# Kernel optimization log

Hardware: AMD Instinct MI355X
Metric: run time of the kernel (lower is better)

The kernel has to match this reference:

```python
import jax, jax.numpy as jnp
import numpy as np

N_NODES = 100000
N_EDGES = 3200000
F_IN = 128
HIDDEN = 16
OUT_DIM = 16
NUM_GRAPHS = 64


def setup_inputs() -> dict:
    key = jax.random.key(0)
    ks = jax.random.split(key, 9)
    x = jax.random.normal(ks[0], (N_NODES, F_IN), dtype=jnp.float32)
    edge_index = jax.random.randint(ks[1], (2, N_EDGES), 0, N_NODES, dtype=jnp.int32)
    batch = jnp.sort(jax.random.randint(ks[2], (N_NODES,), 0, NUM_GRAPHS, dtype=jnp.int32))
    W1 = jax.random.normal(ks[3], (F_IN, HIDDEN), dtype=jnp.float32) * (1.0 / np.sqrt(F_IN))
    b1 = jnp.zeros((HIDDEN,), dtype=jnp.float32)
    W2 = jax.random.normal(ks[4], (HIDDEN, OUT_DIM), dtype=jnp.float32) * (1.0 / np.sqrt(HIDDEN))
    b2 = jnp.zeros((OUT_DIM,), dtype=jnp.float32)
    fc_w = jax.random.normal(ks[5], (OUT_DIM, 1), dtype=jnp.float32) * (1.0 / np.sqrt(OUT_DIM))
    fc_b = jnp.zeros((1,), dtype=jnp.float32)
    return {"x": x, "edge_index": edge_index, "batch": batch,
            "W1": W1, "b1": b1, "W2": W2, "b2": b2, "fc_w": fc_w, "fc_b": fc_b}


def _gcn_conv(x, edge_index, W, b):
    """PyG GCNConv: x' = D^-1/2 (A+I) D^-1/2 (x W) + b (with self-loops)."""
    n = x.shape[0]
    h = x @ W  # transform first (small dim), then propagate
    src, dst = edge_index[0], edge_index[1]
    # degree including the self-loop (+1)
    deg = jax.ops.segment_sum(jnp.ones(src.shape, h.dtype), dst, num_segments=n) + 1.0
    dis = jax.lax.rsqrt(deg)  # deg >= 1 so no zeros
    norm = dis[src] * dis[dst]  # [E]
    agg = jax.ops.segment_sum(h[src] * norm[:, None], dst, num_segments=n)
    # self-loop contribution: norm_ii = dis[i]^2
    return agg + (dis * dis)[:, None] * h + b


def reference(x, edge_index, batch, W1, b1, W2, b2, fc_w, fc_b):
    h = jax.nn.relu(_gcn_conv(x, edge_index, W1, b1))
    # F.dropout(training=False) in eval mode is identity
    h = jax.nn.relu(_gcn_conv(h, edge_index, W2, b2))
    pooled = jax.ops.segment_sum(h, batch, num_segments=NUM_GRAPHS)  # global_add_pool
    return jax.nn.sigmoid(pooled @ fc_w + fc_b)  # [NUM_GRAPHS, 1]
```

## Files before the change

### kernel.cpp

```cpp
#include <hip/hip_runtime.h>
#include <hip/hip_fp16.h>
#include <math.h>

#define N_NODES 100000
#define N_EDGES 3200000
#define F_IN    128
#define NGRAPH  64

#define NB      512
#define BWIDTH  196
#define NPAD    100352
#define BIN_CAP 7200
#define EPB     4096

typedef int   iv4 __attribute__((ext_vector_type(4)));
typedef float fv4 __attribute__((ext_vector_type(4)));
typedef float fv2 __attribute__((ext_vector_type(2)));

#define OFF_BINCUR 0
#define OFF_GZ     512
#define OFF_BBASE  576
#define OFF_DIS    1088
#define OFF_ROWR   (1088 + NPAD)
#define OFF_COL    (1088 + NPAD * 3)
#define OFF_BINNED (OFF_COL + N_EDGES)
#define OFF_HINH   OFF_BINNED
#define OFF_HINH2  (OFF_BINNED + NPAD * 8)

__global__ void zero_k(int* __restrict__ p) {
    p[threadIdx.x] = 0;
}

__global__ void __launch_bounds__(512)
bin_k(const int* __restrict__ ei, int* __restrict__ binCursor,
      int* __restrict__ binned) {
    __shared__ int cntL[NB], cnt2[NB], gbase[NB];
    int tid = threadIdx.x;
    cntL[tid] = 0; cnt2[tid] = 0;
    __syncthreads();
    int myBase = blockIdx.x * EPB + tid * 8;
    bool act = (myBase < N_EDGES);
    int s[8], d[8];
    if (act) {
        const iv4* sp = (const iv4*)(ei + myBase);
        const iv4* dp = (const iv4*)(ei + N_EDGES + myBase);
        iv4 a = __builtin_nontemporal_load(sp);
        iv4 b2 = __builtin_nontemporal_load(sp + 1);
        iv4 c = __builtin_nontemporal_load(dp);
        iv4 e = __builtin_nontemporal_load(dp + 1);
        s[0]=a.x; s[1]=a.y; s[2]=a.z; s[3]=a.w; s[4]=b2.x; s[5]=b2.y; s[6]=b2.z; s[7]=b2.w;
        d[0]=c.x; d[1]=c.y; d[2]=c.z; d[3]=c.w; d[4]=e.x; d[5]=e.y; d[6]=e.z; d[7]=e.w;
#pragma unroll
        for (int k = 0; k < 8; ++k)
            atomicAdd(&cntL[(unsigned)d[k] / BWIDTH], 1);
    }
    __syncthreads();
    gbase[tid] = atomicAdd(&binCursor[tid], cntL[tid]);
    __syncthreads();
    if (act) {
#pragma unroll
        for (int k = 0; k < 8; ++k) {
            int b = (unsigned)d[k] / BWIDTH;
            int off = atomicAdd(&cnt2[b], 1);
            binned[(size_t)b * BIN_CAP + gbase[b] + off] = ((d[k] - b * BWIDTH) << 17) | s[k];
        }
    }
}

__global__ void __launch_bounds__(512)
scanB_k(const int* __restrict__ binCur, int* __restrict__ bucketBase) {
    __shared__ int wsum[8];
    int tid = threadIdx.x;
    int v = binCur[tid];
    int lane = tid & 63, wid = tid >> 6;
    int sc = v;
#pragma unroll
    for (int d = 1; d < 64; d <<= 1) {
        int o = __shfl_up(sc, d);
        if (lane >= d) sc += o;
    }
    if (lane == 63) wsum[wid] = sc;
    __syncthreads();
    int woff = 0;
    for (int w = 0; w < wid; ++w) woff += wsum[w];
    bucketBase[tid] = woff + sc - v;
}

__global__ void __launch_bounds__(512)
sort_k(const int* __restrict__ binCursor, const int* __restrict__ bucketBase,
       const int* __restrict__ binned, float* __restrict__ dis,
       int2* __restrict__ rowRange, int* __restrict__ col) {
    __shared__ int cnt[BWIDTH];
    __shared__ int rowLoc[BWIDTH + 1];
    __shared__ int cur[BWIDTH];
    __shared__ int wsum[8];
    int b = blockIdx.x, tid = threadIdx.x;
    if (tid < BWIDTH) cnt[tid] = 0;
    __syncthreads();
    int n = binCursor[b];
    const int* bb = binned + (size_t)b * BIN_CAP;
    for (int i = tid; i < n; i += 512)
        atomicAdd(&cnt[bb[i] >> 17], 1);
    __syncthreads();
    int base = b * BWIDTH;
    int bw = min(BWIDTH, N_NODES - base);
    if (tid < bw)
        dis[base + tid] = rsqrtf((float)cnt[tid] + 1.0f);
    int a = (tid < BWIDTH) ? cnt[tid] : 0;
    int lane = tid & 63, wid = tid >> 6;
    int sc = a;
#pragma unroll
    for (int d = 1; d < 64; d <<= 1) {
        int o = __shfl_up(sc, d);
        if (lane >= d) sc += o;
    }
    if (lane == 63) wsum[wid] = sc;
    __syncthreads();
    int woff = 0;
    for (int w = 0; w < wid; ++w) woff += wsum[w];
    if (tid < BWIDTH) {
        int excl = woff + sc - a;
        rowLoc[tid] = excl;
        cur[tid] = excl;
    }
    if (tid == 0) rowLoc[BWIDTH] = n;
    __syncthreads();
    int eb = bucketBase[b];
    if (tid < bw) {
        int2 rr; rr.x = eb + rowLoc[tid]; rr.y = eb + rowLoc[tid + 1];
        rowRange[base + tid] = rr;
    }
    for (int i = tid; i < n; i += 512) {
        int p = bb[i];
        int pos = atomicAdd(&cur[p >> 17], 1);
        col[eb + pos] = p & 0x1FFFF;
    }
}

__global__ void transform1_k(const float* __restrict__ x, const float* __restrict__ W,
                             const float* __restrict__ dis, __half* __restrict__ outh) {
    int i = blockIdx.x * blockDim.x + threadIdx.x;
    if (i >= N_NODES) return;
    const fv4* xr = (const fv4*)(x + (size_t)i * F_IN);
    float acc[16];
#pragma unroll
    for (int j = 0; j < 16; ++j) acc[j] = 0.f;
#pragma unroll 4
    for (int k4 = 0; k4 < F_IN / 4; ++k4) {
        fv4 xv = xr[k4];
#pragma unroll
        for (int kk = 0; kk < 4; ++kk) {
            int k = k4 * 4 + kk;
            float xk = xv[kk];
#pragma unroll
            for (int j = 0; j < 16; ++j)
                acc[j] = fmaf(xk, W[k * 16 + j], acc[j]);
        }
    }
    float di = dis[i];
    __half2 t[8];
#pragma unroll
    for (int q = 0; q < 8; ++q)
        t[q] = __floats2half2_rn(di * acc[2 * q], di * acc[2 * q + 1]);
    iv4* o = (iv4*)(outh + (size_t)i * 16);
    o[0] = *(iv4*)&t[0];
    o[1] = *(iv4*)&t[4];
}

__device__ __forceinline__ void gather_row(const __half2* __restrict__ hh,
                                           const int* __restrict__ col,
                                           int e0, int e1, int j,
                                           float& outx, float& outy) {
    float ax0 = 0.f, ay0 = 0.f, ax1 = 0.f, ay1 = 0.f;
    float ax2 = 0.f, ay2 = 0.f, ax3 = 0.f, ay3 = 0.f;
    float bx0 = 0.f, by0 = 0.f, bx1 = 0.f, by1 = 0.f;
    float bx2 = 0.f, by2 = 0.f, bx3 = 0.f, by3 = 0.f;
    int e = e0;
    for (; e + 8 <= e1; e += 8) {
        int myc = col[e + j];
        int s0 = __shfl(myc, 0, 8);
        int s1 = __shfl(myc, 1, 8);
        int s2 = __shfl(myc, 2, 8);
        int s3 = __shfl(myc, 3, 8);
        int s4 = __shfl(myc, 4, 8);
        int s5 = __shfl(myc, 5, 8);
        int s6 = __shfl(myc, 6, 8);
        int s7 = __shfl(myc, 7, 8);
        float2 f0 = __half22float2(hh[s0 * 8 + j]);
        float2 f1 = __half22float2(hh[s1 * 8 + j]);
        float2 f2 = __half22float2(hh[s2 * 8 + j]);
        float2 f3 = __half22float2(hh[s3 * 8 + j]);
        float2 f4 = __half22float2(hh[s4 * 8 + j]);
        float2 f5 = __half22float2(hh[s5 * 8 + j]);
        float2 f6 = __half22float2(hh[s6 * 8 + j]);
        float2 f7 = __half22float2(hh[s7 * 8 + j]);
        ax0 += f0.x; ay0 += f0.y;
        ax1 += f1.x; ay1 += f1.y;
        ax2 += f2.x; ay2 += f2.y;
        ax3 += f3.x; ay3 += f3.y;
        bx0 += f4.x; by0 += f4.y;
        bx1 += f5.x; by1 += f5.y;
        bx2 += f6.x; by2 += f6.y;
        bx3 += f7.x; by3 += f7.y;
    }
    if (e + 4 <= e1) {
        int myc = col[e + (j & 3)];
        int s0 = __shfl(myc, 0, 8);
        int s1 = __shfl(myc, 1, 8);
        int s2 = __shfl(myc, 2, 8);
        int s3 = __shfl(myc, 3, 8);
        float2 f0 = __half22float2(hh[s0 * 8 + j]);
        float2 f1 = __half22float2(hh[s1 * 8 + j]);
        float2 f2 = __half22float2(hh[s2 * 8 + j]);
        float2 f3 = __half22float2(hh[s3 * 8 + j]);
        ax0 += f0.x; ay0 += f0.y;
        ax1 += f1.x; ay1 += f1.y;
        ax2 += f2.x; ay2 += f2.y;
        ax3 += f3.x; ay3 += f3.y;
        e += 4;
    }
    for (; e < e1; ++e) {
        float2 f = __half22float2(hh[col[e] * 8 + j]);
        ax0 += f.x; ay0 += f.y;
    }
    outx = ((ax0 + ax1) + (ax2 + ax3)) + ((bx0 + bx1) + (bx2 + bx3));
    outy = ((ay0 + ay1) + (ay2 + ay3)) + ((by0 + by1) + (by2 + by3));
}

__global__ void prop1_k(const __half* __restrict__ hinh, const float* __restrict__ dis,
                        const int2* __restrict__ rowRange, const int* __restrict__ col,
                        const float* __restrict__ b1, const float* __restrict__ W2,
                        __half* __restrict__ outh2) {
    int gid = blockIdx.x * blockDim.x + threadIdx.x;
    int node = gid >> 3;
    int j = gid & 7;
    if (node >= N_NODES) return;
    int2 rr = rowRange[node];
    const __half2* hh = (const __half2*)hinh;
    float sx, sy;
    gather_row(hh, col, rr.x, rr.y, j, sx, sy);
    float2 self = __half22float2(hh[node * 8 + j]);
    float di = dis[node];
    fv2 bj = ((const fv2*)b1)[j];
    float hx = fmaxf(fmaf(di, sx + self.x, bj.x), 0.f);
    float hy = fmaxf(fmaf(di, sy + self.y, bj.y), 0.f);
    float h1[16];
#pragma unroll
    for (int k = 0; k < 8; ++k) {
        h1[2 * k]     = __shfl(hx, k, 8);
        h1[2 * k + 1] = __shfl(hy, k, 8);
    }
    const fv2* w2 = (const fv2*)W2;
    float o0 = 0.f, o1 = 0.f;
#pragma unroll
    for (int m = 0; m < 16; ++m) {
        fv2 wv = w2[m * 8 + j];
        o0 = fmaf(h1[m], wv.x, o0);
        o1 = fmaf(h1[m], wv.y, o1);
    }
    ((__half2*)outh2)[node * 8 + j] = __floats2half2_rn(di * o0, di * o1);
}

__global__ void __launch_bounds__(256)
prop2_k(const __half* __restrict__ hinh2, const float* __restrict__ dis,
        const int2* __restrict__ rowRange, const int* __restrict__ col,
        const float* __restrict__ b2, const int* __restrict__ batch,
        const float* __restrict__ fcw, float* __restrict__ gz) {
    __shared__ float ldsz[NGRAPH];
    int tid = threadIdx.x;
    if (tid < NGRAPH) ldsz[tid] = 0.f;
    __syncthreads();
    int gid = blockIdx.x * 256 + tid;
    int node = gid >> 3;
    int j = gid & 7;
    int2 rr = rowRange[node];
    const __half2* hh = (const __half2*)hinh2;
    float sx, sy;
    gather_row(hh, col, rr.x, rr.y, j, sx, sy);
    float2 self = __half22float2(hh[node * 8 + j]);
    float di = dis[node];
    fv2 bj = ((const fv2*)b2)[j];
    float hx = fmaxf(fmaf(di, sx + self.x, bj.x), 0.f);
    float hy = fmaxf(fmaf(di, sy + self.y, bj.y), 0.f);
    fv2 fw = ((const fv2*)fcw)[j];
    float s = hx * fw.x + hy * fw.y;
#pragma unroll
    for (int off = 4; off; off >>= 1) s += __shfl_xor(s, off, 8);
    if (j == 0) atomicAdd(&ldsz[batch[node]], s);
    __syncthreads();
    if (tid < NGRAPH) {
        float v = ldsz[tid];
        if (v != 0.f) atomicAdd(&gz[tid], v);
    }
}

__global__ void sig_k(const float* __restrict__ gz, const float* __restrict__ fcb,
                      float* __restrict__ out) {
    int g = threadIdx.x;
    out[g] = 1.0f / (1.0f + expf(-(gz[g] + fcb[0])));
}

extern "C" void kernel_launch(void* const* d_in, const int* in_sizes, int n_in,
                              void* d_out, int out_size, void* d_ws, size_t ws_size,
                              hipStream_t stream) {
    const float* x    = (const float*)d_in[0];
    const int*   ei   = (const int*)d_in[1];
    const int*   batch= (const int*)d_in[2];
    const float* W1   = (const float*)d_in[3];
    const float* b1   = (const float*)d_in[4];
    const float* W2   = (const float*)d_in[5];
    const float* b2   = (const float*)d_in[6];
    const float* fcw  = (const float*)d_in[7];
    const float* fcb  = (const float*)d_in[8];
    float* out = (float*)d_out;

    float* ws = (float*)d_ws;
    int*    binCur   = (int*)(ws + OFF_BINCUR);
    float*  gz       = ws + OFF_GZ;
    int*    bucketBase = (int*)(ws + OFF_BBASE);
    float*  dis      = ws + OFF_DIS;
    int2*   rowRange = (int2*)(ws + OFF_ROWR);
    int*    col      = (int*)(ws + OFF_COL);
    int*    binned   = (int*)(ws + OFF_BINNED);
    __half* hinH     = (__half*)(ws + OFF_HINH);
    __half* hinH2    = (__half*)(ws + OFF_HINH2);

    const int B = 256;
    int gN   = (N_NODES + B - 1) / B;
    int gNP  = (N_NODES * 8 + B - 1) / B;
    int gBin = (N_EDGES + EPB - 1) / EPB;

    zero_k<<<1, 576, 0, stream>>>(binCur);
    bin_k<<<gBin, 512, 0, stream>>>(ei, binCur, binned);
    scanB_k<<<1, 512, 0, stream>>>(binCur, bucketBase);
    sort_k<<<NB, 512, 0, stream>>>(binCur, bucketBase, binned, dis, rowRange, col);

    transform1_k<<<gN, B, 0, stream>>>(x, W1, dis, hinH);
    prop1_k<<<gNP, B, 0, stream>>>(hinH, dis, rowRange, col, b1, W2, hinH2);
    prop2_k<<<gNP, B, 0, stream>>>(hinH2, dis, rowRange, col, b2, batch, fcw, gz);
    sig_k<<<1, NGRAPH, 0, stream>>>(gz, fcb, out);
}
```

Measured before the change: 148.9 us.

## Sort nodes by degree within windows to balance gather work per wavefront

Records per-node in-degree in the sort kernel and adds a windowed counting-sort kernel that builds a permutation grouping nodes of similar degree within 2048-node windows. Both propagation kernels process nodes through this permutation so the eight nodes sharing a wavefront have similar neighbor counts, reducing idle lanes in the gather loop. It adds a kernel launch, an extra indirection load, and less contiguous access to per-node arrays and output rows.

```diff
diff --git a/kernel.cpp b/kernel.cpp
--- a/kernel.cpp
+++ b/kernel.cpp
@@ -12,6 +12,7 @@
 #define NPAD    100352
 #define BIN_CAP 7200
 #define EPB     4096
+#define PWIN    2048
 
 typedef int   iv4 __attribute__((ext_vector_type(4)));
 typedef float fv4 __attribute__((ext_vector_type(4)));
@@ -21,8 +22,10 @@
 #define OFF_GZ     512
 #define OFF_BBASE  576
 #define OFF_DIS    1088
-#define OFF_ROWR   (1088 + NPAD)
-#define OFF_COL    (1088 + NPAD * 3)
+#define OFF_DEG    (1088 + NPAD)
+#define OFF_PERM   (1088 + NPAD * 2)
+#define OFF_ROWR   (1088 + NPAD * 3)
+#define OFF_COL    (1088 + NPAD * 5)
 #define OFF_BINNED (OFF_COL + N_EDGES)
 #define OFF_HINH   OFF_BINNED
 #define OFF_HINH2  (OFF_BINNED + NPAD * 8)
@@ -89,7 +92,7 @@
 __global__ void __launch_bounds__(512)
 sort_k(const int* __restrict__ binCursor, const int* __restrict__ bucketBase,
        const int* __restrict__ binned, float* __restrict__ dis,
-       int2* __restrict__ rowRange, int* __restrict__ col) {
+       int* __restrict__ deg, int2* __restrict__ rowRange, int* __restrict__ col) {
     __shared__ int cnt[BWIDTH];
     __shared__ int rowLoc[BWIDTH + 1];
     __shared__ int cur[BWIDTH];
@@ -104,8 +107,10 @@
     __syncthreads();
     int base = b * BWIDTH;
     int bw = min(BWIDTH, N_NODES - base);
-    if (tid < bw)
+    if (tid < bw) {
         dis[base + tid] = rsqrtf((float)cnt[tid] + 1.0f);
+        deg[base + tid] = cnt[tid];
+    }
     int a = (tid < BWIDTH) ? cnt[tid] : 0;
     int lane = tid & 63, wid = tid >> 6;
     int sc = a;
@@ -134,6 +139,42 @@
         int p = bb[i];
         int pos = atomicAdd(&cur[p >> 17], 1);
         col[eb + pos] = p & 0x1FFFF;
+    }
+}
+
+__global__ void __launch_bounds__(512)
+permW_k(const int* __restrict__ deg, int* __restrict__ perm) {
+    __shared__ int hist[128];
+    int w0 = blockIdx.x * PWIN;
+    int wn = min(PWIN, N_NODES - w0);
+    int tid = threadIdx.x;
+    if (tid < 128) hist[tid] = 0;
+    __syncthreads();
+    int mybin[4];
+#pragma unroll
+    for (int k = 0; k < 4; ++k) {
+        int i = tid * 4 + k;
+        mybin[k] = -1;
+        if (i < wn) {
+            int d = min(deg[w0 + i], 127);
+            mybin[k] = d;
+            atomicAdd(&hist[d], 1);
+        }
+    }
+    __syncthreads();
+    if (tid == 0) {
+        int acc = 0;
+#pragma unroll
+        for (int bN = 0; bN < 128; ++bN) { int c = hist[bN]; hist[bN] = acc; acc += c; }
+    }
+    __syncthreads();
+#pragma unroll
+    for (int k = 0; k < 4; ++k) {
+        int i = tid * 4 + k;
+        if (i < wn) {
+            int pos = atomicAdd(&hist[mybin[k]], 1);
+            perm[w0 + pos] = w0 + i;
+        }
     }
 }
 
@@ -229,12 +270,14 @@
 
 __global__ void prop1_k(const __half* __restrict__ hinh, const float* __restrict__ dis,
                         const int2* __restrict__ rowRange, const int* __restrict__ col,
+                        const int* __restrict__ perm,
                         const float* __restrict__ b1, const float* __restrict__ W2,
                         __half* __restrict__ outh2) {
     int gid = blockIdx.x * blockDim.x + threadIdx.x;
-    int node = gid >> 3;
+    int grp = gid >> 3;
     int j = gid & 7;
-    if (node >= N_NODES) return;
+    if (grp >= N_NODES) return;
+    int node = perm[grp];
     int2 rr = rowRange[node];
     const __half2* hh = (const __half2*)hinh;
     float sx, sy;
@@ -264,6 +307,7 @@
 __global__ void __launch_bounds__(256)
 prop2_k(const __half* __restrict__ hinh2, const float* __restrict__ dis,
         const int2* __restrict__ rowRange, const int* __restrict__ col,
+        const int* __restrict__ perm,
         const float* __restrict__ b2, const int* __restrict__ batch,
         const float* __restrict__ fcw, float* __restrict__ gz) {
     __shared__ float ldsz[NGRAPH];
@@ -271,8 +315,9 @@
     if (tid < NGRAPH) ldsz[tid] = 0.f;
     __syncthreads();
     int gid = blockIdx.x * 256 + tid;
-    int node = gid >> 3;
+    int grp = gid >> 3;
     int j = gid & 7;
+    int node = perm[grp];
     int2 rr = rowRange[node];
     const __half2* hh = (const __half2*)hinh2;
     float sx, sy;
@@ -319,6 +364,8 @@
     float*  gz       = ws + OFF_GZ;
     int*    bucketBase = (int*)(ws + OFF_BBASE);
     float*  dis      = ws + OFF_DIS;
+    int*    deg      = (int*)(ws + OFF_DEG);
+    int*    perm     = (int*)(ws + OFF_PERM);
     int2*   rowRange = (int2*)(ws + OFF_ROWR);
     int*    col      = (int*)(ws + OFF_COL);
     int*    binned   = (int*)(ws + OFF_BINNED);
@@ -329,14 +376,16 @@
     int gN   = (N_NODES + B - 1) / B;
     int gNP  = (N_NODES * 8 + B - 1) / B;
     int gBin = (N_EDGES + EPB - 1) / EPB;
+    int gPW  = (N_NODES + PWIN - 1) / PWIN;
 
     zero_k<<<1, 576, 0, stream>>>(binCur);
     bin_k<<<gBin, 512, 0, stream>>>(ei, binCur, binned);
     scanB_k<<<1, 512, 0, stream>>>(binCur, bucketBase);
-    sort_k<<<NB, 512, 0, stream>>>(binCur, bucketBase, binned, dis, rowRange, col);
+    sort_k<<<NB, 512, 0, stream>>>(binCur, bucketBase, binned, dis, deg, rowRange, col);
+    permW_k<<<gPW, 512, 0, stream>>>(deg, perm);
 
     transform1_k<<<gN, B, 0, stream>>>(x, W1, dis, hinH);
-    prop1_k<<<gNP, B, 0, stream>>>(hinH, dis, rowRange, col, b1, W2, hinH2);
-    prop2_k<<<gNP, B, 0, stream>>>(hinH2, dis, rowRange, col, b2, batch, fcw, gz);
+    prop1_k<<<gNP, B, 0, stream>>>(hinH, dis, rowRange, col, perm, b1, W2, hinH2);
+    prop2_k<<<gNP, B, 0, stream>>>(hinH2, dis, rowRange, col, perm, b2, batch, fcw, gz);
     sig_k<<<1, NGRAPH, 0, stream>>>(gz, fcb, out);
 }
```

Result: slower. 156.9 us (+5.3%).

## Reorder nodes by degree within each bin to balance gather workloads

Applied to the files above, without the earlier changes.

The sort kernel now counting-sorts the nodes of each 196-node bin by in-degree, then emits a permuted row-range array and a nodeOf map. Both propagation kernels walk this permuted order, so the 8-lane groups in a wavefront handle nodes of similar degree. This is meant to cut lane divergence and tail imbalance in the gather loops. In exchange it adds extra LDS passes and barriers in sort_k, an extra indirection load per node, and less locality in the self-feature and dis accesses.

```diff
diff --git a/kernel.cpp b/kernel.cpp
--- a/kernel.cpp
+++ b/kernel.cpp
@@ -21,8 +21,9 @@
 #define OFF_GZ     512
 #define OFF_BBASE  576
 #define OFF_DIS    1088
-#define OFF_ROWR   (1088 + NPAD)
-#define OFF_COL    (1088 + NPAD * 3)
+#define OFF_NODEOF (1088 + NPAD)
+#define OFF_ROWR   (1088 + NPAD * 2)
+#define OFF_COL    (1088 + NPAD * 4)
 #define OFF_BINNED (OFF_COL + N_EDGES)
 #define OFF_HINH   OFF_BINNED
 #define OFF_HINH2  (OFF_BINNED + NPAD * 8)
@@ -89,13 +90,17 @@
 __global__ void __launch_bounds__(512)
 sort_k(const int* __restrict__ binCursor, const int* __restrict__ bucketBase,
        const int* __restrict__ binned, float* __restrict__ dis,
-       int2* __restrict__ rowRange, int* __restrict__ col) {
+       int* __restrict__ nodeOf, int2* __restrict__ rowRangeP, int* __restrict__ col) {
     __shared__ int cnt[BWIDTH];
-    __shared__ int rowLoc[BWIDTH + 1];
+    __shared__ int rank[BWIDTH];
+    __shared__ int nodeOfRank[BWIDTH];
+    __shared__ int rowLoc[BWIDTH];
     __shared__ int cur[BWIDTH];
+    __shared__ int histD[128];
     __shared__ int wsum[8];
     int b = blockIdx.x, tid = threadIdx.x;
     if (tid < BWIDTH) cnt[tid] = 0;
+    if (tid >= 256 && tid < 384) histD[tid - 256] = 0;
     __syncthreads();
     int n = binCursor[b];
     const int* bb = binned + (size_t)b * BIN_CAP;
@@ -103,33 +108,65 @@
         atomicAdd(&cnt[bb[i] >> 17], 1);
     __syncthreads();
     int base = b * BWIDTH;
-    int bw = min(BWIDTH, N_NODES - base);
-    if (tid < bw)
-        dis[base + tid] = rsqrtf((float)cnt[tid] + 1.0f);
-    int a = (tid < BWIDTH) ? cnt[tid] : 0;
-    int lane = tid & 63, wid = tid >> 6;
+    int bw = N_NODES - base;
+    if (bw > BWIDTH) bw = BWIDTH;
+    if (bw < 0) bw = 0;
+    int myDeg = (tid < bw) ? cnt[tid] : 0;
+    int myBin = myDeg > 127 ? 127 : myDeg;
+    if (tid < bw) {
+        dis[base + tid] = rsqrtf((float)myDeg + 1.0f);
+        atomicAdd(&histD[myBin], 1);
+    }
+    __syncthreads();
+    {
+        int hv = (tid < 128) ? histD[tid] : 0;
+        int lane = tid & 63, wid = tid >> 6;
+        int sc = hv;
+#pragma unroll
+        for (int d = 1; d < 64; d <<= 1) {
+            int o = __shfl_up(sc, d);
+            if (lane >= d) sc += o;
+        }
+        if (lane == 63 && wid < 2) wsum[wid] = sc;
+        __syncthreads();
+        if (tid < 128) {
+            int woff = (wid == 1) ? wsum[0] : 0;
+            histD[tid] = woff + sc - hv;
+        }
+    }
+    __syncthreads();
+    if (tid < bw) rank[tid] = atomicAdd(&histD[myBin], 1);
+    __syncthreads();
+    if (tid < bw) nodeOfRank[rank[tid]] = tid;
+    __syncthreads();
+    int a = (tid < bw) ? cnt[nodeOfRank[tid]] : 0;
+    int lane = tid & 63, wid2 = tid >> 6;
     int sc = a;
 #pragma unroll
     for (int d = 1; d < 64; d <<= 1) {
         int o = __shfl_up(sc, d);
         if (lane >= d) sc += o;
     }
-    if (lane == 63) wsum[wid] = sc;
+    if (lane == 63) wsum[wid2] = sc;
     __syncthreads();
     int woff = 0;
-    for (int w = 0; w < wid; ++w) woff += wsum[w];
-    if (tid < BWIDTH) {
-        int excl = woff + sc - a;
-        rowLoc[tid] = excl;
-        cur[tid] = excl;
-    }
-    if (tid == 0) rowLoc[BWIDTH] = n;
+    for (int w = 0; w < wid2; ++w) woff += wsum[w];
+    int excl = woff + sc - a;
+    if (tid < bw) rowLoc[tid] = excl;
     __syncthreads();
     int eb = bucketBase[b];
     if (tid < bw) {
-        int2 rr; rr.x = eb + rowLoc[tid]; rr.y = eb + rowLoc[tid + 1];
-        rowRange[base + tid] = rr;
-    }
+        int q = tid;
+        int t = nodeOfRank[q];
+        int dg = cnt[t];
+        int2 rr; rr.x = eb + rowLoc[q]; rr.y = eb + rowLoc[q] + dg;
+        rowRangeP[base + q] = rr;
+        nodeOf[base + q] = base + t;
+        cur[t] = rowLoc[q];
+    } else if (tid < BWIDTH) {
+        nodeOf[base + tid] = -1;
+    }
+    __syncthreads();
     for (int i = tid; i < n; i += 512) {
         int p = bb[i];
         int pos = atomicAdd(&cur[p >> 17], 1);
@@ -228,14 +265,16 @@
 }
 
 __global__ void prop1_k(const __half* __restrict__ hinh, const float* __restrict__ dis,
-                        const int2* __restrict__ rowRange, const int* __restrict__ col,
+                        const int2* __restrict__ rowRangeP, const int* __restrict__ col,
+                        const int* __restrict__ nodeOf,
                         const float* __restrict__ b1, const float* __restrict__ W2,
                         __half* __restrict__ outh2) {
     int gid = blockIdx.x * blockDim.x + threadIdx.x;
-    int node = gid >> 3;
+    int p = gid >> 3;
     int j = gid & 7;
-    if (node >= N_NODES) return;
-    int2 rr = rowRange[node];
+    int node = nodeOf[p];
+    if (node < 0) return;
+    int2 rr = rowRangeP[p];
     const __half2* hh = (const __half2*)hinh;
     float sx, sy;
     gather_row(hh, col, rr.x, rr.y, j, sx, sy);
@@ -263,7 +302,8 @@
 
 __global__ void __launch_bounds__(256)
 prop2_k(const __half* __restrict__ hinh2, const float* __restrict__ dis,
-        const int2* __restrict__ rowRange, const int* __restrict__ col,
+        const int2* __restrict__ rowRangeP, const int* __restrict__ col,
+        const int* __restrict__ nodeOf,
         const float* __restrict__ b2, const int* __restrict__ batch,
         const float* __restrict__ fcw, float* __restrict__ gz) {
     __shared__ float ldsz[NGRAPH];
@@ -271,22 +311,27 @@
     if (tid < NGRAPH) ldsz[tid] = 0.f;
     __syncthreads();
     int gid = blockIdx.x * 256 + tid;
-    int node = gid >> 3;
+    int p = gid >> 3;
     int j = gid & 7;
-    int2 rr = rowRange[node];
-    const __half2* hh = (const __half2*)hinh2;
-    float sx, sy;
-    gather_row(hh, col, rr.x, rr.y, j, sx, sy);
-    float2 self = __half22float2(hh[node * 8 + j]);
-    float di = dis[node];
-    fv2 bj = ((const fv2*)b2)[j];
-    float hx = fmaxf(fmaf(di, sx + self.x, bj.x), 0.f);
-    float hy = fmaxf(fmaf(di, sy + self.y, bj.y), 0.f);
-    fv2 fw = ((const fv2*)fcw)[j];
-    float s = hx * fw.x + hy * fw.y;
+    int node = nodeOf[p];
+    bool act = (node >= 0);
+    float s = 0.f;
+    if (act) {
+        int2 rr = rowRangeP[p];
+        const __half2* hh = (const __half2*)hinh2;
+        float sx, sy;
+        gather_row(hh, col, rr.x, rr.y, j, sx, sy);
+        float2 self = __half22float2(hh[node * 8 + j]);
+        float di = dis[node];
+        fv2 bj = ((const fv2*)b2)[j];
+        float hx = fmaxf(fmaf(di, sx + self.x, bj.x), 0.f);
+        float hy = fmaxf(fmaf(di, sy + self.y, bj.y), 0.f);
+        fv2 fw = ((const fv2*)fcw)[j];
+        s = hx * fw.x + hy * fw.y;
+    }
 #pragma unroll
     for (int off = 4; off; off >>= 1) s += __shfl_xor(s, off, 8);
-    if (j == 0) atomicAdd(&ldsz[batch[node]], s);
+    if (act && j == 0) atomicAdd(&ldsz[batch[node]], s);
     __syncthreads();
     if (tid < NGRAPH) {
         float v = ldsz[tid];
@@ -319,7 +364,8 @@
     float*  gz       = ws + OFF_GZ;
     int*    bucketBase = (int*)(ws + OFF_BBASE);
     float*  dis      = ws + OFF_DIS;
-    int2*   rowRange = (int2*)(ws + OFF_ROWR);
+    int*    nodeOf   = (int*)(ws + OFF_NODEOF);
+    int2*   rowRangeP= (int2*)(ws + OFF_ROWR);
     int*    col      = (int*)(ws + OFF_COL);
     int*    binned   = (int*)(ws + OFF_BINNED);
     __half* hinH     = (__half*)(ws + OFF_HINH);
@@ -327,16 +373,16 @@
 
     const int B = 256;
     int gN   = (N_NODES + B - 1) / B;
-    int gNP  = (N_NODES * 8 + B - 1) / B;
+    int gNP  = NPAD * 8 / B;
     int gBin = (N_EDGES + EPB - 1) / EPB;
 
     zero_k<<<1, 576, 0, stream>>>(binCur);
     bin_k<<<gBin, 512, 0, stream>>>(ei, binCur, binned);
     scanB_k<<<1, 512, 0, stream>>>(binCur, bucketBase);
-    sort_k<<<NB, 512, 0, stream>>>(binCur, bucketBase, binned, dis, rowRange, col);
+    sort_k<<<NB, 512, 0, stream>>>(binCur, bucketBase, binned, dis, nodeOf, rowRangeP, col);
 
     transform1_k<<<gN, B, 0, stream>>>(x, W1, dis, hinH);
-    prop1_k<<<gNP, B, 0, stream>>>(hinH, dis, rowRange, col, b1, W2, hinH2);
-    prop2_k<<<gNP, B, 0, stream>>>(hinH2, dis, rowRange, col, b2, batch, fcw, gz);
+    prop1_k<<<gNP, B, 0, stream>>>(hinH, dis, rowRangeP, col, nodeOf, b1, W2, hinH2);
+    prop2_k<<<gNP, B, 0, stream>>>(hinH2, dis, rowRangeP, col, nodeOf, b2, batch, fcw, gz);
     sig_k<<<1, NGRAPH, 0, stream>>>(gz, fcb, out);
 }
```

Result: no change. 149.8 us (+0.6%).
